# Kernel tuning notes

Measured on AMD Instinct MI355X. Metric: run time of the kernel, lower is better.

The kernel has to match this reference:

```python
import jax, jax.numpy as jnp
import numpy as np

HID = 512
HEADS = 8
HEAD_DIM = HID // HEADS
B, S = 2, 4096


def setup_inputs() -> dict:
    key = jax.random.key(0)
    ks = jax.random.split(key, 11)
    sc = 0.02
    return {
        "query": jax.random.normal(ks[0], (B, S, HID), jnp.float32),
        "key": jax.random.normal(ks[1], (B, S, HID), jnp.float32),
        "value": jax.random.normal(ks[2], (B, S, HID), jnp.float32),
        "Wq": jax.random.normal(ks[3], (HID, HID), jnp.float32) * sc,
        "bq": jax.random.normal(ks[4], (HID,), jnp.float32) * sc,
        "Wk": jax.random.normal(ks[5], (HID, HID), jnp.float32) * sc,
        "bk": jax.random.normal(ks[6], (HID,), jnp.float32) * sc,
        "Wv": jax.random.normal(ks[7], (HID, HID), jnp.float32) * sc,
        "bv": jax.random.normal(ks[8], (HID,), jnp.float32) * sc,
        "Wo": jax.random.normal(ks[9], (HID, HID), jnp.float32) * sc,
        "bo": jax.random.normal(ks[10], (HID,), jnp.float32) * sc,
    }


def reference(query, key, value, Wq, bq, Wk, bk, Wv, bv, Wo, bo):
    b, s, _ = query.shape
    scale = jnp.sqrt(jnp.float32(HEAD_DIM))
    # projections (nn.Linear: x @ W.T + b)
    Q = query @ Wq.T + bq
    K = key @ Wk.T + bk
    V = value @ Wv.T + bv
    # split heads: [b, h, s, d]
    Q = Q.reshape(b, s, HEADS, HEAD_DIM).transpose(0, 2, 1, 3)
    K = K.reshape(b, s, HEADS, HEAD_DIM).transpose(0, 2, 1, 3)
    V = V.reshape(b, s, HEADS, HEAD_DIM).transpose(0, 2, 1, 3)
    # scaled dot-product attention (mask=None, dropout in eval mode = identity)
    energy = jnp.einsum('bhqd,bhkd->bhqk', Q, K) / scale
    attention = jax.nn.softmax(energy, axis=-1)
    x = jnp.einsum('bhqk,bhkd->bhqd', attention, V)
    x = x.transpose(0, 2, 1, 3).reshape(b, s, HID)
    return x @ Wo.T + bo
```

## Files before the change

### kernel.cpp

```cpp
#include <hip/hip_runtime.h>
#include <stdint.h>

#define HID 512
#define NH 8
#define HD 64
#define BATCH 2
#define SEQ 4096
#define M_TOT (BATCH*SEQ)
#define NBH (BATCH*NH)

typedef __attribute__((ext_vector_type(8))) short short8;
typedef __attribute__((ext_vector_type(4))) short short4v;
typedef __attribute__((ext_vector_type(4))) float floatx4;
typedef unsigned short u16;

__device__ inline u16 f2bf(float x) {
  unsigned u = __builtin_bit_cast(unsigned, x);
  unsigned r = u + 0x7fff + ((u >> 16) & 1);
  return (u16)(r >> 16);
}

__device__ inline unsigned pack_bf16(float a, float b) {
  unsigned ua = __builtin_bit_cast(unsigned, a) + 0x8000u;
  unsigned ub = __builtin_bit_cast(unsigned, b) + 0x8000u;
  return __builtin_amdgcn_perm(ub, ua, 0x07060302u);
}

__device__ inline void gll16(const void* g, void* l) {
  __builtin_amdgcn_global_load_lds((const __attribute__((address_space(1))) void*)g,
                                   (__attribute__((address_space(3))) void*)l, 16, 0, 0);
}


__global__ void cvt_all(const float* __restrict__ q, const float* __restrict__ k,
                        const float* __restrict__ v, const float* __restrict__ wq,
                        const float* __restrict__ wk, const float* __restrict__ wv,
                        const float* __restrict__ wo,
                        u16* __restrict__ xq, u16* __restrict__ xk,
                        u16* __restrict__ xv, u16* __restrict__ wb) {
  const int seg = blockIdx.y;
  const size_t NX = (size_t)M_TOT * HID;
  const size_t NW = (size_t)HID * HID;
  const float* src; u16* dst; int n;
  if (seg < 3) {
    src = (seg == 0) ? q : ((seg == 1) ? k : v);
    dst = (seg == 0) ? xq : ((seg == 1) ? xk : xv);
    n = (int)NX;
  } else {
    int w = seg - 3;
    src = (w == 0) ? wq : ((w == 1) ? wk : ((w == 2) ? wv : wo));
    dst = wb + (size_t)w * NW;
    n = (int)NW;
  }
  int i = ((int)blockIdx.x * (int)blockDim.x + (int)threadIdx.x) * 4;
  if (i >= n) return;
  const float4 val = *(const float4*)(src + i);
  union { uint2 u; u16 h[4]; } pk;
  pk.h[0] = f2bf(val.x); pk.h[1] = f2bf(val.y);
  pk.h[2] = f2bf(val.z); pk.h[3] = f2bf(val.w);
  *(uint2*)(dst + i) = pk.u;
}

__global__ __launch_bounds__(256) void gemm_qkv(
    const u16* __restrict__ Xq, const u16* __restrict__ Xk, const u16* __restrict__ Xv,
    const u16* __restrict__ Wb,
    const float* __restrict__ bq, const float* __restrict__ bk, const float* __restrict__ bv,
    u16* __restrict__ Qp, u16* __restrict__ Kp, u16* __restrict__ Vt) {
  const int z = blockIdx.z;
  const u16* X = (z == 0) ? Xq : ((z == 1) ? Xk : Xv);
  const u16* W = Wb + (size_t)z * (HID * HID);
  const float* bias = (z == 0) ? bq : ((z == 1) ? bk : bv);

  __shared__ u16 As[128 * 32];
  __shared__ u16 Bs[128 * 32];

  const int tid = threadIdx.x;
  const int wid = tid >> 6, lane = tid & 63;
  const int wm = wid >> 1, wn = wid & 1;
  const int quad = lane >> 4, l16 = lane & 15;
  const int m0 = (int)blockIdx.x * 128, n0 = (int)blockIdx.y * 128;
  const int srow = lane >> 2;
  const int scol = (lane & 3) * 8;

  floatx4 acc[4][4];
#pragma unroll
  for (int i = 0; i < 4; i++)
#pragma unroll
    for (int j = 0; j < 4; j++) acc[i][j] = floatx4{0.f, 0.f, 0.f, 0.f};

  for (int k0 = 0; k0 < HID; k0 += 32) {
#pragma unroll
    for (int r = 0; r < 2; r++) {
      int row = r * 64 + wid * 16 + srow;
      gll16(X + (size_t)(m0 + row) * HID + k0 + scol, &As[(r * 64 + wid * 16) * 32]);
      gll16(W + (size_t)(n0 + row) * HID + k0 + scol, &Bs[(r * 64 + wid * 16) * 32]);
    }
    __syncthreads();
    short8 af[4], bf[4];
#pragma unroll
    for (int mt = 0; mt < 4; mt++)
      af[mt] = *(const short8*)&As[(wm * 64 + mt * 16 + l16) * 32 + quad * 8];
#pragma unroll
    for (int nt = 0; nt < 4; nt++)
      bf[nt] = *(const short8*)&Bs[(wn * 64 + nt * 16 + l16) * 32 + quad * 8];
#pragma unroll
    for (int mt = 0; mt < 4; mt++)
#pragma unroll
      for (int nt = 0; nt < 4; nt++)
        acc[mt][nt] = __builtin_amdgcn_mfma_f32_16x16x32_bf16(af[mt], bf[nt], acc[mt][nt], 0, 0, 0);
    __syncthreads();
  }

#pragma unroll
  for (int mt = 0; mt < 4; mt++) {
#pragma unroll
    for (int nt = 0; nt < 4; nt++) {
      int ncol = n0 + wn * 64 + nt * 16 + l16;
      float bias_v = bias[ncol];
      int h = ncol >> 6, d = ncol & 63;
#pragma unroll
      for (int r = 0; r < 4; r++) {
        int mrow = m0 + wm * 64 + mt * 16 + quad * 4 + r;
        float v = acc[mt][nt][r] + bias_v;
        int b = mrow >> 12, s = mrow & (SEQ - 1);
        size_t base = (size_t)(b * NH + h) * SEQ * HD;
        if (z == 2) {
          size_t idx = base + (size_t)(s >> 4) * 1024 + (d >> 4) * 256 + ((s >> 2) & 3) * 64 + (d & 15) * 4 + (s & 3);
          Vt[idx] = f2bf(v);
        } else {
          size_t idx = base + (size_t)(s >> 4) * 1024 + (d >> 3) * 128 + (s & 15) * 8 + (d & 7);
          if (z == 0) Qp[idx] = f2bf(v * 0.18033688f);
          else        Kp[idx] = f2bf(v);
        }
      }
    }
  }
}

__global__ __launch_bounds__(256) void gemm_out(
    const u16* __restrict__ X, const u16* __restrict__ W,
    const float* __restrict__ bias, float* __restrict__ out) {
  __shared__ u16 As[128 * 32];
  __shared__ u16 Bs[128 * 32];

  const int tid = threadIdx.x;
  const int wid = tid >> 6, lane = tid & 63;
  const int wm = wid >> 1, wn = wid & 1;
  const int quad = lane >> 4, l16 = lane & 15;
  const int m0 = (int)blockIdx.x * 128, n0 = (int)blockIdx.y * 128;
  const int srow = lane >> 2;
  const int scol = (lane & 3) * 8;

  floatx4 acc[4][4];
#pragma unroll
  for (int i = 0; i < 4; i++)
#pragma unroll
    for (int j = 0; j < 4; j++) acc[i][j] = floatx4{0.f, 0.f, 0.f, 0.f};

  for (int k0 = 0; k0 < HID; k0 += 32) {
#pragma unroll
    for (int r = 0; r < 2; r++) {
      int row = r * 64 + wid * 16 + srow;
      gll16(X + (size_t)(m0 + row) * HID + k0 + scol, &As[(r * 64 + wid * 16) * 32]);
      gll16(W + (size_t)(n0 + row) * HID + k0 + scol, &Bs[(r * 64 + wid * 16) * 32]);
    }
    __syncthreads();
    short8 af[4], bf[4];
#pragma unroll
    for (int mt = 0; mt < 4; mt++)
      af[mt] = *(const short8*)&As[(wm * 64 + mt * 16 + l16) * 32 + quad * 8];
#pragma unroll
    for (int nt = 0; nt < 4; nt++)
      bf[nt] = *(const short8*)&Bs[(wn * 64 + nt * 16 + l16) * 32 + quad * 8];
#pragma unroll
    for (int mt = 0; mt < 4; mt++)
#pragma unroll
      for (int nt = 0; nt < 4; nt++)
        acc[mt][nt] = __builtin_amdgcn_mfma_f32_16x16x32_bf16(af[mt], bf[nt], acc[mt][nt], 0, 0, 0);
    __syncthreads();
  }

#pragma unroll
  for (int mt = 0; mt < 4; mt++) {
#pragma unroll
    for (int nt = 0; nt < 4; nt++) {
      int ncol = n0 + wn * 64 + nt * 16 + l16;
      float bias_v = bias[ncol];
#pragma unroll
      for (int r = 0; r < 4; r++) {
        int mrow = m0 + wm * 64 + mt * 16 + quad * 4 + r;
        out[(size_t)mrow * HID + ncol] = acc[mt][nt][r] + bias_v;
      }
    }
  }
}

__global__ __launch_bounds__(256) void attn_kernel(
    const u16* __restrict__ Qp, const u16* __restrict__ Kp,
    const u16* __restrict__ Vt, float* __restrict__ Op, float* __restrict__ Lp) {
  const int bh = blockIdx.y;
  const int sp = blockIdx.z;
  const int q0 = (int)blockIdx.x * 128;
  const u16* Qh = Qp + (size_t)bh * SEQ * HD;
  const u16* Kh = Kp + (size_t)bh * SEQ * HD;
  const u16* Vh = Vt + (size_t)bh * SEQ * HD;

  const int tid = threadIdx.x;
  const int wid = tid >> 6, lane = tid & 63;
  const int quad = lane >> 4, l16 = lane & 15;

  short8 qf[2][2];
#pragma unroll
  for (int kq = 0; kq < 2; kq++)
#pragma unroll
    for (int n = 0; n < 2; n++)
      qf[kq][n] = *(const short8*)(Qh + (size_t)(q0 / 16 + wid * 2 + n) * 1024 + (kq * 4 + quad) * 128 + l16 * 8);

  float l_part[2] = {0.f, 0.f};
  floatx4 o[2][4];
#pragma unroll
  for (int m = 0; m < 2; m++)
#pragma unroll
    for (int dt = 0; dt < 4; dt++) o[m][dt] = floatx4{0.f, 0.f, 0.f, 0.f};

  const int kv_lo = sp * (SEQ / 2), kv_hi = kv_lo + SEQ / 2;
  for (int kv0 = kv_lo; kv0 < kv_hi; kv0 += 64) {
#pragma unroll
    for (int t = 0; t < 4; t++) {
      const int kt = (kv0 >> 4) + t;
      short8 ak0 = *(const short8*)(Kh + (size_t)kt * 1024 + (0 * 4 + quad) * 128 + l16 * 8);
      short8 ak1 = *(const short8*)(Kh + (size_t)kt * 1024 + (1 * 4 + quad) * 128 + l16 * 8);
      short4v vf[4];
#pragma unroll
      for (int dt = 0; dt < 4; dt++)
        vf[dt] = *(const short4v*)(Vh + (size_t)kt * 1024 + dt * 256 + quad * 64 + l16 * 4);

      floatx4 st[2];
      st[0] = __builtin_amdgcn_mfma_f32_16x16x32_bf16(ak0, qf[0][0], floatx4{0.f,0.f,0.f,0.f}, 0, 0, 0);
      st[1] = __builtin_amdgcn_mfma_f32_16x16x32_bf16(ak0, qf[0][1], floatx4{0.f,0.f,0.f,0.f}, 0, 0, 0);
      st[0] = __builtin_amdgcn_mfma_f32_16x16x32_bf16(ak1, qf[1][0], st[0], 0, 0, 0);
      st[1] = __builtin_amdgcn_mfma_f32_16x16x32_bf16(ak1, qf[1][1], st[1], 0, 0, 0);

#pragma unroll
      for (int n = 0; n < 2; n++) {
        float p0 = __builtin_amdgcn_exp2f(st[n][0]);
        float p1 = __builtin_amdgcn_exp2f(st[n][1]);
        float p2 = __builtin_amdgcn_exp2f(st[n][2]);
        float p3 = __builtin_amdgcn_exp2f(st[n][3]);
        l_part[n] += (p0 + p1) + (p2 + p3);
        union { unsigned u[2]; short4v s; } pk;
        pk.u[0] = pack_bf16(p0, p1);
        pk.u[1] = pack_bf16(p2, p3);
#pragma unroll
        for (int dt = 0; dt < 4; dt++)
          o[n][dt] = __builtin_amdgcn_mfma_f32_16x16x16bf16_1k(pk.s, vf[dt], o[n][dt], 0, 0, 0);
      }
    }
  }

#pragma unroll
  for (int n = 0; n < 2; n++) {
    l_part[n] += __shfl_xor(l_part[n], 16);
    l_part[n] += __shfl_xor(l_part[n], 32);
  }
  float* Oph = Op + (size_t)(sp * NBH + bh) * SEQ * HD;
  float* Lph = Lp + (size_t)(sp * NBH + bh) * SEQ;
  if (quad == 0) {
#pragma unroll
    for (int n = 0; n < 2; n++)
      Lph[q0 + wid * 32 + n * 16 + l16] = l_part[n];
  }
#pragma unroll
  for (int m = 0; m < 2; m++) {
#pragma unroll
    for (int r = 0; r < 4; r++) {
      int s = q0 + wid * 32 + m * 16 + quad * 4 + r;
#pragma unroll
      for (int dt = 0; dt < 4; dt++)
        Oph[(size_t)s * HD + dt * 16 + l16] = o[m][dt][r];
    }
  }
}

__global__ __launch_bounds__(256) void combine_kernel(
    const float* __restrict__ Op, const float* __restrict__ Lp, u16* __restrict__ Xo) {
  int idx = (int)blockIdx.x * 256 + (int)threadIdx.x;
  int e = idx * 4;
  int bh = e >> 18;
  int rem = e & 262143;
  int q = rem >> 6, d = rem & 63;
  size_t i0 = ((size_t)bh * SEQ + q) * HD + d;
  size_t i1 = ((size_t)(NBH + bh) * SEQ + q) * HD + d;
  float4 a = *(const float4*)(Op + i0);
  float4 c = *(const float4*)(Op + i1);
  float inv = 1.f / (Lp[bh * SEQ + q] + Lp[(NBH + bh) * SEQ + q]);
  int b = bh >> 3, h = bh & 7;
  u16* dst = Xo + ((size_t)(b * SEQ + q)) * HID + h * HD + d;
  union { uint2 u; u16 hh[4]; } pk;
  pk.hh[0] = f2bf((a.x + c.x) * inv);
  pk.hh[1] = f2bf((a.y + c.y) * inv);
  pk.hh[2] = f2bf((a.z + c.z) * inv);
  pk.hh[3] = f2bf((a.w + c.w) * inv);
  *(uint2*)dst = pk.u;
}

extern "C" void kernel_launch(void* const* d_in, const int* in_sizes, int n_in,
                              void* d_out, int out_size, void* d_ws, size_t ws_size,
                              hipStream_t stream) {
  const float* q  = (const float*)d_in[0];
  const float* k  = (const float*)d_in[1];
  const float* v  = (const float*)d_in[2];
  const float* Wq = (const float*)d_in[3];
  const float* bq = (const float*)d_in[4];
  const float* Wk = (const float*)d_in[5];
  const float* bk = (const float*)d_in[6];
  const float* Wv = (const float*)d_in[7];
  const float* bv = (const float*)d_in[8];
  const float* Wo = (const float*)d_in[9];
  const float* bo = (const float*)d_in[10];

  u16* wsb = (u16*)d_ws;
  const size_t NW = (size_t)HID * HID;
  const size_t NX = (size_t)M_TOT * HID;
  u16* Wb = wsb;
  u16* Xq = wsb + 4 * NW;
  u16* Xk = Xq + NX;
  u16* Xv = Xk + NX;
  u16* Qp = Xv + NX;
  u16* Kp = Qp + NX;
  u16* Vt = Kp + NX;
  u16* Xo = Vt + NX;
  float* Op = (float*)(Xo + NX);
  float* Lp = Op + (size_t)2 * NBH * SEQ * HD;

  dim3 blk(256);
  cvt_all<<<dim3(4096, 7), blk, 0, stream>>>(q, k, v, Wq, Wk, Wv, Wo, Xq, Xk, Xv, Wb);

  gemm_qkv<<<dim3(64, 4, 3), blk, 0, stream>>>(Xq, Xk, Xv, Wb, bq, bk, bv, Qp, Kp, Vt);
  attn_kernel<<<dim3(32, NBH, 2), blk, 0, stream>>>(Qp, Kp, Vt, Op, Lp);
  combine_kernel<<<dim3(4096), blk, 0, stream>>>(Op, Lp, Xo);
  gemm_out<<<dim3(64, 4), blk, 0, stream>>>(Xo, Wb + 3 * NW, bo, (float*)d_out);
}
```

Measured before the change: 256.1 us.

## Split attention KV range four ways and store bf16 partial outputs

Raises the KV split from 2 to 4, doubling the attention grid to 2048 blocks for better occupancy on the many CUs. Partial outputs are stored as bf16 instead of fp32 to cut partial-output traffic, and the combine kernel sums four partials. It also adds a min-8-blocks launch bound hint. Risks are extra combine reads and bf16 rounding of the unnormalized partials.

```diff
diff --git a/kernel.cpp b/kernel.cpp
--- a/kernel.cpp
+++ b/kernel.cpp
@@ -8,6 +8,7 @@
 #define SEQ 4096
 #define M_TOT (BATCH*SEQ)
 #define NBH (BATCH*NH)
+#define SPLITK 4
 
 typedef __attribute__((ext_vector_type(8))) short short8;
 typedef __attribute__((ext_vector_type(4))) short short4v;
@@ -18,6 +19,11 @@
   unsigned u = __builtin_bit_cast(unsigned, x);
   unsigned r = u + 0x7fff + ((u >> 16) & 1);
   return (u16)(r >> 16);
+}
+
+__device__ inline float bf2f(u16 h) {
+  unsigned u = ((unsigned)h) << 16;
+  return __builtin_bit_cast(float, u);
 }
 
 __device__ inline unsigned pack_bf16(float a, float b) {
@@ -195,9 +201,9 @@
   }
 }
 
-__global__ __launch_bounds__(256) void attn_kernel(
+__global__ __launch_bounds__(256, 8) void attn_kernel(
     const u16* __restrict__ Qp, const u16* __restrict__ Kp,
-    const u16* __restrict__ Vt, float* __restrict__ Op, float* __restrict__ Lp) {
+    const u16* __restrict__ Vt, u16* __restrict__ Opb, float* __restrict__ Lp) {
   const int bh = blockIdx.y;
   const int sp = blockIdx.z;
   const int q0 = (int)blockIdx.x * 128;
@@ -223,7 +229,7 @@
 #pragma unroll
     for (int dt = 0; dt < 4; dt++) o[m][dt] = floatx4{0.f, 0.f, 0.f, 0.f};
 
-  const int kv_lo = sp * (SEQ / 2), kv_hi = kv_lo + SEQ / 2;
+  const int kv_lo = sp * (SEQ / SPLITK), kv_hi = kv_lo + SEQ / SPLITK;
   for (int kv0 = kv_lo; kv0 < kv_hi; kv0 += 64) {
 #pragma unroll
     for (int t = 0; t < 4; t++) {
@@ -263,7 +269,7 @@
     l_part[n] += __shfl_xor(l_part[n], 16);
     l_part[n] += __shfl_xor(l_part[n], 32);
   }
-  float* Oph = Op + (size_t)(sp * NBH + bh) * SEQ * HD;
+  u16* Oph = Opb + (size_t)(sp * NBH + bh) * SEQ * HD;
   float* Lph = Lp + (size_t)(sp * NBH + bh) * SEQ;
   if (quad == 0) {
 #pragma unroll
@@ -277,30 +283,36 @@
       int s = q0 + wid * 32 + m * 16 + quad * 4 + r;
 #pragma unroll
       for (int dt = 0; dt < 4; dt++)
-        Oph[(size_t)s * HD + dt * 16 + l16] = o[m][dt][r];
+        Oph[(size_t)s * HD + dt * 16 + l16] = f2bf(o[m][dt][r]);
     }
   }
 }
 
 __global__ __launch_bounds__(256) void combine_kernel(
-    const float* __restrict__ Op, const float* __restrict__ Lp, u16* __restrict__ Xo) {
+    const u16* __restrict__ Opb, const float* __restrict__ Lp, u16* __restrict__ Xo) {
   int idx = (int)blockIdx.x * 256 + (int)threadIdx.x;
   int e = idx * 4;
   int bh = e >> 18;
   int rem = e & 262143;
   int q = rem >> 6, d = rem & 63;
-  size_t i0 = ((size_t)bh * SEQ + q) * HD + d;
-  size_t i1 = ((size_t)(NBH + bh) * SEQ + q) * HD + d;
-  float4 a = *(const float4*)(Op + i0);
-  float4 c = *(const float4*)(Op + i1);
-  float inv = 1.f / (Lp[bh * SEQ + q] + Lp[(NBH + bh) * SEQ + q]);
+  float acc0 = 0.f, acc1 = 0.f, acc2 = 0.f, acc3 = 0.f, lsum = 0.f;
+#pragma unroll
+  for (int sp = 0; sp < SPLITK; sp++) {
+    size_t i = ((size_t)(sp * NBH + bh) * SEQ + q) * HD + d;
+    union { uint2 u; u16 h[4]; } pk;
+    pk.u = *(const uint2*)(Opb + i);
+    acc0 += bf2f(pk.h[0]); acc1 += bf2f(pk.h[1]);
+    acc2 += bf2f(pk.h[2]); acc3 += bf2f(pk.h[3]);
+    lsum += Lp[(size_t)(sp * NBH + bh) * SEQ + q];
+  }
+  float inv = 1.f / lsum;
   int b = bh >> 3, h = bh & 7;
   u16* dst = Xo + ((size_t)(b * SEQ + q)) * HID + h * HD + d;
   union { uint2 u; u16 hh[4]; } pk;
-  pk.hh[0] = f2bf((a.x + c.x) * inv);
-  pk.hh[1] = f2bf((a.y + c.y) * inv);
-  pk.hh[2] = f2bf((a.z + c.z) * inv);
-  pk.hh[3] = f2bf((a.w + c.w) * inv);
+  pk.hh[0] = f2bf(acc0 * inv);
+  pk.hh[1] = f2bf(acc1 * inv);
+  pk.hh[2] = f2bf(acc2 * inv);
+  pk.hh[3] = f2bf(acc3 * inv);
   *(uint2*)dst = pk.u;
 }
 
@@ -330,14 +342,14 @@
   u16* Kp = Qp + NX;
   u16* Vt = Kp + NX;
   u16* Xo = Vt + NX;
-  float* Op = (float*)(Xo + NX);
-  float* Lp = Op + (size_t)2 * NBH * SEQ * HD;
+  u16* Opb = Xo + NX;
+  float* Lp = (float*)(Opb + (size_t)SPLITK * NBH * SEQ * HD);
 
   dim3 blk(256);
   cvt_all<<<dim3(4096, 7), blk, 0, stream>>>(q, k, v, Wq, Wk, Wv, Wo, Xq, Xk, Xv, Wb);
 
   gemm_qkv<<<dim3(64, 4, 3), blk, 0, stream>>>(Xq, Xk, Xv, Wb, bq, bk, bv, Qp, Kp, Vt);
-  attn_kernel<<<dim3(32, NBH, 2), blk, 0, stream>>>(Qp, Kp, Vt, Op, Lp);
-  combine_kernel<<<dim3(4096), blk, 0, stream>>>(Op, Lp, Xo);
+  attn_kernel<<<dim3(32, NBH, SPLITK), blk, 0, stream>>>(Qp, Kp, Vt, Opb, Lp);
+  combine_kernel<<<dim3(4096), blk, 0, stream>>>(Opb, Lp, Xo);
   gemm_out<<<dim3(64, 4), blk, 0, stream>>>(Xo, Wb + 3 * NW, bo, (float*)d_out);
 }
```

Measured after the change: 826.0 us. 223% more time.
